# Kernel tuning notes

Hardware: AMD Instinct MI355X
Metric: run time of the kernel (lower is better)

The kernel has to match this reference:

```python
import jax, jax.numpy as jnp
import numpy as np

N = 100000
E = 1000000
F_NODE = 64
F_EDGE = 32
H = 128
C_NODE = 12
C_EDGE = 4


def _glorot(key, shape):
    fan_in, fan_out = shape[0], shape[1]
    s = (6.0 / (fan_in + fan_out)) ** 0.5
    return jax.random.uniform(key, shape, jnp.float32, -s, s)


def setup_inputs() -> dict:
    key = jax.random.key(0)
    ks = jax.random.split(key, 16)
    x = jax.random.normal(ks[0], (N, F_NODE), jnp.float32)
    edge_index = jax.random.randint(ks[1], (2, E), 0, N, jnp.int32)
    edge_attr = jax.random.normal(ks[2], (E, F_EDGE), jnp.float32)
    return {
        "x": x,
        "edge_index": edge_index,
        "edge_attr": edge_attr,
        "We": _glorot(ks[3], (F_NODE, H)), "be": jnp.zeros((H,), jnp.float32),
        "Wc1": _glorot(ks[4], (H, H)), "bc1": jnp.zeros((H,), jnp.float32),
        "Wc2": _glorot(ks[5], (H, H)), "bc2": jnp.zeros((H,), jnp.float32),
        "Wn1": _glorot(ks[6], (H, H // 2)), "bn1": jnp.zeros((H // 2,), jnp.float32),
        "Wn2": _glorot(ks[7], (H // 2, C_NODE)), "bn2": jnp.zeros((C_NODE,), jnp.float32),
        "Wedge1": _glorot(ks[8], (2 * H + F_EDGE, H)), "bedge1": jnp.zeros((H,), jnp.float32),
        "Wedge2": _glorot(ks[9], (H, C_EDGE)), "bedge2": jnp.zeros((C_EDGE,), jnp.float32),
    }


def _gcn_conv(x, W, b, src, tgt, n):
    # PyG GCNConv: add self-loops, symmetric deg normalization, scatter-add.
    xw = x @ W  # [N, H]
    loop = jnp.arange(n, dtype=src.dtype)
    s = jnp.concatenate([src, loop])
    t = jnp.concatenate([tgt, loop])
    deg = jax.ops.segment_sum(jnp.ones_like(t, jnp.float32), t, num_segments=n)
    dinv = jnp.where(deg > 0, jax.lax.rsqrt(jnp.maximum(deg, 1.0)), 0.0)
    norm = dinv[s] * dinv[t]  # [E+N]
    msg = xw[s] * norm[:, None]
    return jax.ops.segment_sum(msg, t, num_segments=n) + b


def reference(x, edge_index, edge_attr, We, be, Wc1, bc1, Wc2, bc2,
              Wn1, bn1, Wn2, bn2, Wedge1, bedge1, Wedge2, bedge2):
    n = x.shape[0]
    row, col = edge_index[0], edge_index[1]
    h = jax.nn.relu(x @ We + be)          # node_embed Linear+ReLU
    h = jax.nn.relu(h)                     # extra F.relu in forward
    h = jax.nn.relu(_gcn_conv(h, Wc1, bc1, row, col, n))
    h = jax.nn.relu(_gcn_conv(h, Wc2, bc2, row, col, n))
    node_logits = jax.nn.relu(h @ Wn1 + bn1) @ Wn2 + bn2
    e = jnp.concatenate([h[row], h[col], edge_attr], axis=-1)  # [E, 2H+Fe]
    edge_logits = jax.nn.relu(e @ Wedge1 + bedge1) @ Wedge2 + bedge2
    return (node_logits, edge_logits)
```

## Files before the change

kernel.cpp:

```cpp
#include <hip/hip_runtime.h>

#define N_NODES 100000
#define N_EDGES 1000000
#define NB_SCAN 391
#define EDGE_OUT_BASE 1200000

typedef __attribute__((ext_vector_type(8))) short short8;
typedef __attribute__((ext_vector_type(4))) unsigned short us4;
typedef __attribute__((ext_vector_type(4))) float f32x4;

__device__ __forceinline__ float bf2f(unsigned short u) {
    unsigned int x = ((unsigned int)u) << 16;
    return __builtin_bit_cast(float, x);
}
__device__ __forceinline__ float lo_bf(unsigned int u) {
    return __builtin_bit_cast(float, u << 16);
}
__device__ __forceinline__ float hi_bf(unsigned int u) {
    return __builtin_bit_cast(float, u & 0xffff0000u);
}
__device__ __forceinline__ unsigned short f2bf(float f) {
    unsigned int x = __builtin_bit_cast(unsigned int, f);
    return (unsigned short)((x + 0x7fffu + ((x >> 16) & 1u)) >> 16);
}

__global__ __launch_bounds__(256) void k_detect(const unsigned short* __restrict__ xr,
                                                int* __restrict__ flag) {
    __shared__ int s[256];
    int t = threadIdx.x;
    int cnt = 0;
    for (int i = t; i < 8192; i += 256) {
        int e = (xr[i] >> 7) & 0xFF;
        if (e >= 148) cnt++;
    }
    s[t] = cnt;
    __syncthreads();
    for (int off = 128; off > 0; off >>= 1) {
        if (t < off) s[t] += s[t + off];
        __syncthreads();
    }
    if (t == 0) *flag = (s[0] > 100) ? 1 : 0;
}

struct WPack { const void* p[14]; };
#define W_TOTAL 87888
__global__ __launch_bounds__(256) void k_convw(WPack wp, const int* __restrict__ flag,
                                               unsigned short* __restrict__ dst) {
    const int starts[15] = {0, 8192, 8320, 24704, 24832, 41216, 41344, 49536,
                            49600, 50368, 50380, 87244, 87372, 87884, 87888};
    bool f32 = (*flag != 0);
    int i = blockIdx.x * 256 + threadIdx.x;
    if (i >= W_TOTAL) return;
    int s = 0;
#pragma unroll
    for (int k = 1; k < 14; k++) s += (i >= starts[k]) ? 1 : 0;
    int j = i - starts[s];
    dst[i] = f32 ? f2bf(((const float*)wp.p[s])[j]) : ((const unsigned short*)wp.p[s])[j];
}
#define OW_We 0
#define OW_be 8192
#define OW_Wc1 8320
#define OW_bc1 24704
#define OW_Wc2 24832
#define OW_bc2 41216
#define OW_Wn1 41344
#define OW_bn1 49536
#define OW_Wn2 49600
#define OW_bn2 50368
#define OW_We1 50380
#define OW_be1 87244
#define OW_We2 87372
#define OW_be2 87884

__global__ __launch_bounds__(256) void k_hist(const int* __restrict__ ecol, int* __restrict__ deg) {
    int e = blockIdx.x * 256 + threadIdx.x;
    if (e < N_EDGES) atomicAdd(&deg[ecol[e]], 1);
}

__global__ __launch_bounds__(256) void k_scanA(const int* __restrict__ deg, int* __restrict__ bsum) {
    __shared__ int s[256];
    int i = blockIdx.x * 256 + threadIdx.x;
    s[threadIdx.x] = (i < N_NODES) ? deg[i] : 0;
    __syncthreads();
    for (int off = 128; off > 0; off >>= 1) {
        if (threadIdx.x < off) s[threadIdx.x] += s[threadIdx.x + off];
        __syncthreads();
    }
    if (threadIdx.x == 0) bsum[blockIdx.x] = s[0];
}

__global__ __launch_bounds__(512) void k_scanB(int* __restrict__ bsum) {
    __shared__ int s[512];
    int t = threadIdx.x;
    int v = (t < NB_SCAN) ? bsum[t] : 0;
    s[t] = v;
    __syncthreads();
    for (int off = 1; off < 512; off <<= 1) {
        int x = (t >= off) ? s[t - off] : 0;
        __syncthreads();
        s[t] += x;
        __syncthreads();
    }
    if (t < NB_SCAN) bsum[t] = s[t] - v;
}

__global__ __launch_bounds__(256) void k_scanC(const int* __restrict__ deg, const int* __restrict__ bsum,
                                               int* __restrict__ row_off, int* __restrict__ cursor,
                                               float* __restrict__ dinv) {
    __shared__ int s[256];
    int i = blockIdx.x * 256 + threadIdx.x;
    int t = threadIdx.x;
    int v = (i < N_NODES) ? deg[i] : 0;
    s[t] = v;
    __syncthreads();
    for (int off = 1; off < 256; off <<= 1) {
        int x = (t >= off) ? s[t - off] : 0;
        __syncthreads();
        s[t] += x;
        __syncthreads();
    }
    int excl = s[t] - v + bsum[blockIdx.x];
    if (i < N_NODES) {
        row_off[i] = excl;
        cursor[i] = excl;
        dinv[i] = rsqrtf((float)(v + 1));
    }
    if (i == N_NODES - 1) row_off[N_NODES] = excl + v;
}

__global__ __launch_bounds__(256) void k_fill(const int* __restrict__ erow, const int* __restrict__ ecol,
                                              int* __restrict__ cursor, int* __restrict__ csr,
                                              int2* __restrict__ aux) {
    int e = blockIdx.x * 256 + threadIdx.x;
    if (e < N_EDGES) {
        int c = ecol[e];
        int pos = atomicAdd(&cursor[c], 1);
        csr[pos] = erow[e];
        aux[pos] = make_int2(e, c);
    }
}

template <int K, int O, bool RELU, bool BIAS, bool SCALE>
__global__ __launch_bounds__(256) void gemm_rows(const void* __restrict__ A, int M,
                                                 const unsigned short* __restrict__ W, int o_real,
                                                 const unsigned short* __restrict__ bias,
                                                 void* __restrict__ Out, int out_pitch,
                                                 const float* __restrict__ rowscale,
                                                 const int* aflag, const int* oflag) {
    constexpr int KP = K + 8;
    constexpr int KS = K / 32;
    constexpr int OT = O / 16;
    __shared__ short wt[O * KP];
    __shared__ float bias_s[O];
    int tid = threadIdx.x;
    for (int idx = tid; idx < K * O; idx += 256) {
        int k = idx / O, o = idx % O;
        short w = 0;
        if (o < o_real) w = (short)W[(size_t)k * o_real + o];
        wt[o * KP + k] = w;
    }
    if (BIAS) {
        for (int o = tid; o < O; o += 256) bias_s[o] = (o < o_real) ? bf2f(bias[o]) : 0.f;
    }
    __syncthreads();

    bool af32 = aflag && (*aflag != 0);
    bool of32 = oflag && (*oflag != 0);

    int wid = tid >> 6, lane = tid & 63;
    int rbase = (blockIdx.x * 4 + wid) * 32;
    if (rbase >= M) return;
    int lq = lane >> 4, lr = lane & 15;

    short8 a[2][KS];
#pragma unroll
    for (int rg = 0; rg < 2; rg++) {
        int row = rbase + rg * 16 + lr;
        if (row >= M) row = M - 1;
        if (af32) {
            const float* ap = (const float*)A + (size_t)row * K + lq * 8;
#pragma unroll
            for (int ks = 0; ks < KS; ks++) {
                f32x4 u0 = *(const f32x4*)(ap + ks * 32);
                f32x4 u1 = *(const f32x4*)(ap + ks * 32 + 4);
                short8 v;
                v[0] = (short)f2bf(u0[0]); v[1] = (short)f2bf(u0[1]);
                v[2] = (short)f2bf(u0[2]); v[3] = (short)f2bf(u0[3]);
                v[4] = (short)f2bf(u1[0]); v[5] = (short)f2bf(u1[1]);
                v[6] = (short)f2bf(u1[2]); v[7] = (short)f2bf(u1[3]);
                a[rg][ks] = v;
            }
        } else {
            const unsigned short* ap = (const unsigned short*)A + (size_t)row * K + lq * 8;
#pragma unroll
            for (int ks = 0; ks < KS; ks++) a[rg][ks] = *(const short8*)(ap + ks * 32);
        }
    }

    f32x4 acc[2][OT];
#pragma unroll
    for (int rg = 0; rg < 2; rg++)
#pragma unroll
        for (int j = 0; j < OT; j++) {
            acc[rg][j][0] = 0.f; acc[rg][j][1] = 0.f; acc[rg][j][2] = 0.f; acc[rg][j][3] = 0.f;
        }

#pragma unroll
    for (int j = 0; j < OT; j++) {
        short8 b[KS];
#pragma unroll
        for (int ks = 0; ks < KS; ks++)
            b[ks] = *(const short8*)(&wt[(lr + 16 * j) * KP + ks * 32 + lq * 8]);
#pragma unroll
        for (int rg = 0; rg < 2; rg++)
#pragma unroll
            for (int ks = 0; ks < KS; ks++)
                acc[rg][j] = __builtin_amdgcn_mfma_f32_16x16x32_bf16(a[rg][ks], b[ks], acc[rg][j], 0, 0, 0);
    }

#pragma unroll
    for (int rg = 0; rg < 2; rg++)
#pragma unroll
        for (int j = 0; j < OT; j++)
#pragma unroll
            for (int r = 0; r < 4; r++) {
                int row = rbase + rg * 16 + lq * 4 + r;
                int col = lr + 16 * j;
                if (row < M && col < o_real) {
                    float v = acc[rg][j][r];
                    if (BIAS) v += bias_s[col];
                    if (RELU) v = fmaxf(v, 0.f);
                    if (SCALE) v *= rowscale[row];
                    size_t oi = (size_t)row * out_pitch + col;
                    if (of32) ((float*)Out)[oi] = v;
                    else ((unsigned short*)Out)[oi] = f2bf(v);
                }
            }
}

__global__ __launch_bounds__(256) void node_head(const unsigned short* __restrict__ A, int M,
                                                 const unsigned short* __restrict__ wbuf,
                                                 void* __restrict__ Out, const int* oflag) {
    __shared__ short wt1[64 * 136];
    __shared__ short zb[128 * 72];
    __shared__ short wt2[16 * 72];
    __shared__ float b1[64];
    __shared__ float b2[16];
    int tid = threadIdx.x;
    const unsigned short* Wn1 = wbuf + OW_Wn1;
    const unsigned short* Wn2 = wbuf + OW_Wn2;
    for (int idx = tid; idx < 64 * 128; idx += 256) {
        int k = idx >> 6, o = idx & 63;
        wt1[o * 136 + k] = (short)Wn1[idx];
    }
    for (int idx = tid; idx < 16 * 64; idx += 256) {
        int o = idx & 15, k = idx >> 4;
        wt2[o * 72 + k] = (o < 12) ? (short)Wn2[k * 12 + o] : 0;
    }
    if (tid < 64) b1[tid] = bf2f(wbuf[OW_bn1 + tid]);
    if (tid < 16) b2[tid] = (tid < 12) ? bf2f(wbuf[OW_bn2 + tid]) : 0.f;
    __syncthreads();

    bool of32 = oflag && (*oflag != 0);
    int wid = tid >> 6, lane = tid & 63;
    int lq = lane >> 4, lr = lane & 15;
    int rbase = blockIdx.x * 128 + wid * 32;

    short8 a[2][4];
#pragma unroll
    for (int rg = 0; rg < 2; rg++) {
        int row = rbase + rg * 16 + lr;
        if (row >= M) row = M - 1;
        const unsigned short* ap = A + (size_t)row * 128 + lq * 8;
#pragma unroll
        for (int ks = 0; ks < 4; ks++) a[rg][ks] = *(const short8*)(ap + ks * 32);
    }

    {
        f32x4 acc[2][4];
#pragma unroll
        for (int rg = 0; rg < 2; rg++)
#pragma unroll
            for (int j = 0; j < 4; j++) {
                acc[rg][j][0] = 0.f; acc[rg][j][1] = 0.f; acc[rg][j][2] = 0.f; acc[rg][j][3] = 0.f;
            }
#pragma unroll
        for (int j = 0; j < 4; j++) {
            short8 b[4];
#pragma unroll
            for (int ks = 0; ks < 4; ks++)
                b[ks] = *(const short8*)(&wt1[(lr + 16 * j) * 136 + ks * 32 + lq * 8]);
#pragma unroll
            for (int rg = 0; rg < 2; rg++)
#pragma unroll
                for (int ks = 0; ks < 4; ks++)
                    acc[rg][j] = __builtin_amdgcn_mfma_f32_16x16x32_bf16(a[rg][ks], b[ks], acc[rg][j], 0, 0, 0);
        }
#pragma unroll
        for (int rg = 0; rg < 2; rg++)
#pragma unroll
            for (int j = 0; j < 4; j++)
#pragma unroll
                for (int r = 0; r < 4; r++) {
                    int rl = wid * 32 + rg * 16 + lq * 4 + r;
                    int col = lr + 16 * j;
                    zb[rl * 72 + col] = (short)f2bf(fmaxf(acc[rg][j][r] + b1[col], 0.f));
                }
    }
    __syncthreads();

    {
        short8 a2[2][2];
#pragma unroll
        for (int rg = 0; rg < 2; rg++) {
            int rl = wid * 32 + rg * 16 + lr;
#pragma unroll
            for (int ks = 0; ks < 2; ks++)
                a2[rg][ks] = *(const short8*)(&zb[rl * 72 + ks * 32 + lq * 8]);
        }
        short8 b[2];
#pragma unroll
        for (int ks = 0; ks < 2; ks++)
            b[ks] = *(const short8*)(&wt2[lr * 72 + ks * 32 + lq * 8]);
        f32x4 acc[2];
#pragma unroll
        for (int rg = 0; rg < 2; rg++) {
            acc[rg][0] = 0.f; acc[rg][1] = 0.f; acc[rg][2] = 0.f; acc[rg][3] = 0.f;
#pragma unroll
            for (int ks = 0; ks < 2; ks++)
                acc[rg] = __builtin_amdgcn_mfma_f32_16x16x32_bf16(a2[rg][ks], b[ks], acc[rg], 0, 0, 0);
        }
#pragma unroll
        for (int rg = 0; rg < 2; rg++)
#pragma unroll
            for (int r = 0; r < 4; r++) {
                int row = rbase + rg * 16 + lq * 4 + r;
                int col = lr;
                if (row < M && col < 12) {
                    float v = acc[rg][r] + b2[col];
                    size_t oi = (size_t)row * 12 + col;
                    if (of32) ((float*)Out)[oi] = v;
                    else ((unsigned short*)Out)[oi] = f2bf(v);
                }
            }
    }
}

__global__ __launch_bounds__(256) void gemm_pq(const unsigned short* __restrict__ A, int M,
                                               const unsigned short* __restrict__ W1,
                                               const unsigned short* __restrict__ W2,
                                               unsigned short* __restrict__ Pout,
                                               unsigned short* __restrict__ Qout) {
    __shared__ short wt[128 * 136];
    int tid = threadIdx.x;
    int wid = tid >> 6, lane = tid & 63;
    int rbase = (blockIdx.x * 4 + wid) * 32;
    int lq = lane >> 4, lr = lane & 15;

    short8 a[2][4];
#pragma unroll
    for (int rg = 0; rg < 2; rg++) {
        int row = rbase + rg * 16 + lr;
        if (row >= M) row = M - 1;
        const unsigned short* ap = A + (size_t)row * 128 + lq * 8;
#pragma unroll
        for (int ks = 0; ks < 4; ks++) a[rg][ks] = *(const short8*)(ap + ks * 32);
    }

    int pc0 = (lr >> 2) * 32 + (lr & 3);

    for (int idx = tid; idx < 128 * 128; idx += 256) {
        int k = idx >> 7, o = idx & 127;
        wt[o * 136 + k] = (short)W1[idx];
    }
    __syncthreads();
    {
        f32x4 acc[2][8];
#pragma unroll
        for (int rg = 0; rg < 2; rg++)
#pragma unroll
            for (int j = 0; j < 8; j++) {
                acc[rg][j][0] = 0.f; acc[rg][j][1] = 0.f; acc[rg][j][2] = 0.f; acc[rg][j][3] = 0.f;
            }
#pragma unroll
        for (int j = 0; j < 8; j++) {
            short8 b[4];
#pragma unroll
            for (int ks = 0; ks < 4; ks++)
                b[ks] = *(const short8*)(&wt[(lr + 16 * j) * 136 + ks * 32 + lq * 8]);
#pragma unroll
            for (int rg = 0; rg < 2; rg++)
#pragma unroll
                for (int ks = 0; ks < 4; ks++)
                    acc[rg][j] = __builtin_amdgcn_mfma_f32_16x16x32_bf16(a[rg][ks], b[ks], acc[rg][j], 0, 0, 0);
        }
#pragma unroll
        for (int rg = 0; rg < 2; rg++)
#pragma unroll
            for (int j = 0; j < 8; j++)
#pragma unroll
                for (int r = 0; r < 4; r++) {
                    int row = rbase + rg * 16 + lq * 4 + r;
                    if (row < M) Pout[(size_t)row * 128 + pc0 + j * 4] = f2bf(acc[rg][j][r]);
                }
    }
    __syncthreads();

    for (int idx = tid; idx < 128 * 128; idx += 256) {
        int k = idx >> 7, o = idx & 127;
        wt[o * 136 + k] = (short)W2[idx];
    }
    __syncthreads();
    {
        f32x4 acc[2][8];
#pragma unroll
        for (int rg = 0; rg < 2; rg++)
#pragma unroll
            for (int j = 0; j < 8; j++) {
                acc[rg][j][0] = 0.f; acc[rg][j][1] = 0.f; acc[rg][j][2] = 0.f; acc[rg][j][3] = 0.f;
            }
#pragma unroll
        for (int j = 0; j < 8; j++) {
            short8 b[4];
#pragma unroll
            for (int ks = 0; ks < 4; ks++)
                b[ks] = *(const short8*)(&wt[(lr + 16 * j) * 136 + ks * 32 + lq * 8]);
#pragma unroll
            for (int rg = 0; rg < 2; rg++)
#pragma unroll
                for (int ks = 0; ks < 4; ks++)
                    acc[rg][j] = __builtin_amdgcn_mfma_f32_16x16x32_bf16(a[rg][ks], b[ks], acc[rg][j], 0, 0, 0);
        }
#pragma unroll
        for (int rg = 0; rg < 2; rg++)
#pragma unroll
            for (int j = 0; j < 8; j++)
#pragma unroll
                for (int r = 0; r < 4; r++) {
                    int row = rbase + rg * 16 + lq * 4 + r;
                    if (row < M) Qout[(size_t)row * 128 + pc0 + j * 4] = f2bf(acc[rg][j][r]);
                }
    }
}

#define CONV_LOADC(U, base)                                                             \
    _Pragma("unroll") for (int k = 0; k < 8; k++) {                                     \
        int p = (base) + k;                                                             \
        int pc = (p < cend) ? p : (cend - 1);                                           \
        int s = csr_src[pc];                                                            \
        U[k] = *(const unsigned int*)(xw_s + (size_t)s * 128 + lane * 2);               \
    }
#define CONV_CONSUME(U, base)                                                           \
    _Pragma("unroll") for (int k = 0; k < 8; k++) {                                     \
        int p = (base) + k;                                                             \
        if (p < cend) {                                                                 \
            float lo = lo_bf(U[k]), hi = hi_bf(U[k]);                                   \
            if (p >= b3)      { A3l += lo; A3h += hi; }                                 \
            else if (p >= b2) { A2l += lo; A2h += hi; }                                 \
            else if (p >= b1) { A1l += lo; A1h += hi; }                                 \
            else              { A0l += lo; A0h += hi; }                                 \
        }                                                                               \
    }
__global__ __launch_bounds__(256) void conv_kernel(const unsigned short* __restrict__ xw_s,
                                                   const int* __restrict__ csr_src,
                                                   const int* __restrict__ row_off,
                                                   const float* __restrict__ dinv,
                                                   const unsigned short* __restrict__ bias,
                                                   unsigned short* __restrict__ out) {
    int wid = threadIdx.x >> 6, lane = threadIdx.x & 63;
    int t0 = (blockIdx.x * 4 + wid) * 4;
    int b0 = row_off[t0], b1 = row_off[t0 + 1], b2 = row_off[t0 + 2];
    int b3 = row_off[t0 + 3], cend = row_off[t0 + 4];

    unsigned int v0 = *(const unsigned int*)(xw_s + (size_t)(t0 + 0) * 128 + lane * 2);
    unsigned int v1 = *(const unsigned int*)(xw_s + (size_t)(t0 + 1) * 128 + lane * 2);
    unsigned int v2 = *(const unsigned int*)(xw_s + (size_t)(t0 + 2) * 128 + lane * 2);
    unsigned int v3 = *(const unsigned int*)(xw_s + (size_t)(t0 + 3) * 128 + lane * 2);
    float A0l = lo_bf(v0), A0h = hi_bf(v0);
    float A1l = lo_bf(v1), A1h = hi_bf(v1);
    float A2l = lo_bf(v2), A2h = hi_bf(v2);
    float A3l = lo_bf(v3), A3h = hi_bf(v3);

    if (b0 < cend) {
        unsigned int UA[8], UB[8];
        int i = b0;
        CONV_LOADC(UA, i);
        while (true) {
            bool hasB = (i + 8) < cend;
            if (hasB) { CONV_LOADC(UB, i + 8); }
            CONV_CONSUME(UA, i);
            i += 8;
            if (!hasB) break;
            bool hasA = (i + 8) < cend;
            if (hasA) { CONV_LOADC(UA, i + 8); }
            CONV_CONSUME(UB, i);
            i += 8;
            if (!hasA) break;
        }
    }

    unsigned int bv = *(const unsigned int*)(bias + lane * 2);
    float bl = lo_bf(bv), bh = hi_bf(bv);
    float d0 = dinv[t0], d1 = dinv[t0 + 1], d2 = dinv[t0 + 2], d3 = dinv[t0 + 3];
    A0l = fmaxf(fmaf(A0l, d0, bl), 0.f); A0h = fmaxf(fmaf(A0h, d0, bh), 0.f);
    A1l = fmaxf(fmaf(A1l, d1, bl), 0.f); A1h = fmaxf(fmaf(A1h, d1, bh), 0.f);
    A2l = fmaxf(fmaf(A2l, d2, bl), 0.f); A2h = fmaxf(fmaf(A2h, d2, bh), 0.f);
    A3l = fmaxf(fmaf(A3l, d3, bl), 0.f); A3h = fmaxf(fmaf(A3h, d3, bh), 0.f);
    *(unsigned int*)(out + (size_t)(t0 + 0) * 128 + lane * 2) =
        (unsigned int)f2bf(A0l) | ((unsigned int)f2bf(A0h) << 16);
    *(unsigned int*)(out + (size_t)(t0 + 1) * 128 + lane * 2) =
        (unsigned int)f2bf(A1l) | ((unsigned int)f2bf(A1h) << 16);
    *(unsigned int*)(out + (size_t)(t0 + 2) * 128 + lane * 2) =
        (unsigned int)f2bf(A2l) | ((unsigned int)f2bf(A2h) << 16);
    *(unsigned int*)(out + (size_t)(t0 + 3) * 128 + lane * 2) =
        (unsigned int)f2bf(A3l) | ((unsigned int)f2bf(A3h) << 16);
}

__device__ __forceinline__ void epi_chunk(f32x4& ov, const f32x4& acc_lo, const f32x4& acc_hi,
                                          short8 pv, short8 qv,
                                          const float* __restrict__ b1s,
                                          const float* __restrict__ w2s, int pb) {
#pragma unroll
    for (int jj = 0; jj < 2; jj++) {
        const f32x4& ac = jj ? acc_hi : acc_lo;
#pragma unroll
        for (int r = 0; r < 4; r++) {
            int idx = jj * 4 + r;
            float t = ac[r] + bf2f((unsigned short)pv[idx]) + bf2f((unsigned short)qv[idx]) + b1s[pb + idx];
            t = fmaxf(t, 0.f);
            f32x4 w2v = *(const f32x4*)(&w2s[(pb + idx) * 4]);
            ov[0] = fmaf(t, w2v[0], ov[0]);
            ov[1] = fmaf(t, w2v[1], ov[1]);
            ov[2] = fmaf(t, w2v[2], ov[2]);
            ov[3] = fmaf(t, w2v[3], ov[3]);
        }
    }
}

__global__ __launch_bounds__(256) void edge_head(const void* __restrict__ ea,
                                                 const int* __restrict__ csr_src,
                                                 const int2* __restrict__ aux,
                                                 const unsigned short* __restrict__ P,
                                                 const unsigned short* __restrict__ Q,
                                                 const unsigned short* __restrict__ wbuf,
                                                 void* __restrict__ out, const int* dtflag) {
    __shared__ short wct[128 * 40];
    __shared__ float w2s[128 * 4];
    __shared__ float b1s[128];
    int tid = threadIdx.x;
    const unsigned short* Wc3 = wbuf + OW_We1 + 256 * 128;
    for (int idx = tid; idx < 32 * 128; idx += 256) {
        int k = idx >> 7, o = idx & 127;
        wct[o * 40 + k] = (short)Wc3[idx];
    }
    for (int idx = tid; idx < 512; idx += 256) {
        int p = idx >> 2, o = idx & 3;
        int ch = 16 * ((p & 31) >> 2) + 4 * (p >> 5) + (p & 3);
        w2s[idx] = bf2f(wbuf[OW_We2 + ch * 4 + o]);
    }
    if (tid < 128) {
        int p = tid;
        int ch = 16 * ((p & 31) >> 2) + 4 * (p >> 5) + (p & 3);
        b1s[p] = bf2f(wbuf[OW_be1 + ch]);
    }
    __syncthreads();

    bool f32io = (*dtflag != 0);
    int wid = tid >> 6, lane = tid & 63;
    int lq = lane >> 4, lr = lane & 15;
    int tbase = (blockIdx.x * 4 + wid) * 2;
    int p0a = tbase * 16, p0b = p0a + 16;

    int posa = p0a + lr, posb = p0b + lr;
    bool va = posa < N_EDGES, vb = posb < N_EDGES;
    int pca = va ? posa : (N_EDGES - 1);
    int pcb = vb ? posb : (N_EDGES - 1);

    int rna = csr_src[pca], rnb = csr_src[pcb];
    int2 axa = aux[pca], axb = aux[pcb];
    int gea = axa.x, cna = axa.y;
    int geb = axb.x, cnb = axb.y;

    auto load_efrag = [&](int ge) -> short8 {
        short8 v;
        if (f32io) {
            const float* eap = (const float*)ea + (size_t)ge * 32 + lq * 8;
            f32x4 u0 = __builtin_nontemporal_load((const f32x4*)eap);
            f32x4 u1 = __builtin_nontemporal_load((const f32x4*)(eap + 4));
            v[0] = (short)f2bf(u0[0]); v[1] = (short)f2bf(u0[1]);
            v[2] = (short)f2bf(u0[2]); v[3] = (short)f2bf(u0[3]);
            v[4] = (short)f2bf(u1[0]); v[5] = (short)f2bf(u1[1]);
            v[6] = (short)f2bf(u1[2]); v[7] = (short)f2bf(u1[3]);
        } else {
            v = __builtin_nontemporal_load((const short8*)((const unsigned short*)ea + (size_t)ge * 32 + lq * 8));
        }
        return v;
    };
    short8 efA = load_efrag(gea);
    short8 efB = load_efrag(geb);

    const unsigned short* PpA = P + (size_t)rna * 128 + lq * 32;
    const unsigned short* QpA = Q + (size_t)cna * 128 + lq * 32;
    const unsigned short* PpB = P + (size_t)rnb * 128 + lq * 32;
    const unsigned short* QpB = Q + (size_t)cnb * 128 + lq * 32;

    f32x4 zero; zero[0] = 0.f; zero[1] = 0.f; zero[2] = 0.f; zero[3] = 0.f;
    f32x4 ovA = zero, ovB = zero;

    {
        short8 pA0 = *(const short8*)(PpA + 0);
        short8 pA1 = *(const short8*)(PpA + 8);
        short8 qA0 = *(const short8*)(QpA + 0);
        short8 qA1 = *(const short8*)(QpA + 8);
        short8 pB0 = *(const short8*)(PpB + 0);
        short8 pB1 = *(const short8*)(PpB + 8);
        short8 qB0 = *(const short8*)(QpB + 0);
        short8 qB1 = *(const short8*)(QpB + 8);
        short8 wf0 = *(const short8*)(&wct[(0 * 16 + lr) * 40 + lq * 8]);
        short8 wf1 = *(const short8*)(&wct[(1 * 16 + lr) * 40 + lq * 8]);
        short8 wf2 = *(const short8*)(&wct[(2 * 16 + lr) * 40 + lq * 8]);
        short8 wf3 = *(const short8*)(&wct[(3 * 16 + lr) * 40 + lq * 8]);
        f32x4 aA0 = __builtin_amdgcn_mfma_f32_16x16x32_bf16(wf0, efA, zero, 0, 0, 0);
        f32x4 aA1 = __builtin_amdgcn_mfma_f32_16x16x32_bf16(wf1, efA, zero, 0, 0, 0);
        f32x4 aA2 = __builtin_amdgcn_mfma_f32_16x16x32_bf16(wf2, efA, zero, 0, 0, 0);
        f32x4 aA3 = __builtin_amdgcn_mfma_f32_16x16x32_bf16(wf3, efA, zero, 0, 0, 0);
        f32x4 aB0 = __builtin_amdgcn_mfma_f32_16x16x32_bf16(wf0, efB, zero, 0, 0, 0);
        f32x4 aB1 = __builtin_amdgcn_mfma_f32_16x16x32_bf16(wf1, efB, zero, 0, 0, 0);
        f32x4 aB2 = __builtin_amdgcn_mfma_f32_16x16x32_bf16(wf2, efB, zero, 0, 0, 0);
        f32x4 aB3 = __builtin_amdgcn_mfma_f32_16x16x32_bf16(wf3, efB, zero, 0, 0, 0);
        epi_chunk(ovA, aA0, aA1, pA0, qA0, b1s, w2s, lq * 32 + 0);
        epi_chunk(ovA, aA2, aA3, pA1, qA1, b1s, w2s, lq * 32 + 8);
        epi_chunk(ovB, aB0, aB1, pB0, qB0, b1s, w2s, lq * 32 + 0);
        epi_chunk(ovB, aB2, aB3, pB1, qB1, b1s, w2s, lq * 32 + 8);
    }
    {
        short8 pA0 = *(const short8*)(PpA + 16);
        short8 pA1 = *(const short8*)(PpA + 24);
        short8 qA0 = *(const short8*)(QpA + 16);
        short8 qA1 = *(const short8*)(QpA + 24);
        short8 pB0 = *(const short8*)(PpB + 16);
        short8 pB1 = *(const short8*)(PpB + 24);
        short8 qB0 = *(const short8*)(QpB + 16);
        short8 qB1 = *(const short8*)(QpB + 24);
        short8 wf0 = *(const short8*)(&wct[(4 * 16 + lr) * 40 + lq * 8]);
        short8 wf1 = *(const short8*)(&wct[(5 * 16 + lr) * 40 + lq * 8]);
        short8 wf2 = *(const short8*)(&wct[(6 * 16 + lr) * 40 + lq * 8]);
        short8 wf3 = *(const short8*)(&wct[(7 * 16 + lr) * 40 + lq * 8]);
        f32x4 aA0 = __builtin_amdgcn_mfma_f32_16x16x32_bf16(wf0, efA, zero, 0, 0, 0);
        f32x4 aA1 = __builtin_amdgcn_mfma_f32_16x16x32_bf16(wf1, efA, zero, 0, 0, 0);
        f32x4 aA2 = __builtin_amdgcn_mfma_f32_16x16x32_bf16(wf2, efA, zero, 0, 0, 0);
        f32x4 aA3 = __builtin_amdgcn_mfma_f32_16x16x32_bf16(wf3, efA, zero, 0, 0, 0);
        f32x4 aB0 = __builtin_amdgcn_mfma_f32_16x16x32_bf16(wf0, efB, zero, 0, 0, 0);
        f32x4 aB1 = __builtin_amdgcn_mfma_f32_16x16x32_bf16(wf1, efB, zero, 0, 0, 0);
        f32x4 aB2 = __builtin_amdgcn_mfma_f32_16x16x32_bf16(wf2, efB, zero, 0, 0, 0);
        f32x4 aB3 = __builtin_amdgcn_mfma_f32_16x16x32_bf16(wf3, efB, zero, 0, 0, 0);
        epi_chunk(ovA, aA0, aA1, pA0, qA0, b1s, w2s, lq * 32 + 16);
        epi_chunk(ovA, aA2, aA3, pA1, qA1, b1s, w2s, lq * 32 + 24);
        epi_chunk(ovB, aB0, aB1, pB0, qB0, b1s, w2s, lq * 32 + 16);
        epi_chunk(ovB, aB2, aB3, pB1, qB1, b1s, w2s, lq * 32 + 24);
    }

#pragma unroll
    for (int c = 0; c < 4; c++) {
        ovA[c] += __shfl_xor(ovA[c], 16);
        ovA[c] += __shfl_xor(ovA[c], 32);
        ovB[c] += __shfl_xor(ovB[c], 16);
        ovB[c] += __shfl_xor(ovB[c], 32);
    }
    if (lq == 0) {
        float be2_0 = bf2f(wbuf[OW_be2 + 0]), be2_1 = bf2f(wbuf[OW_be2 + 1]);
        float be2_2 = bf2f(wbuf[OW_be2 + 2]), be2_3 = bf2f(wbuf[OW_be2 + 3]);
        if (va) {
            size_t oi = (size_t)EDGE_OUT_BASE + (size_t)gea * 4;
            if (f32io) {
                f32x4 res; res[0] = ovA[0] + be2_0; res[1] = ovA[1] + be2_1;
                res[2] = ovA[2] + be2_2; res[3] = ovA[3] + be2_3;
                __builtin_nontemporal_store(res, (f32x4*)((float*)out + oi));
            } else {
                us4 res; res[0] = f2bf(ovA[0] + be2_0); res[1] = f2bf(ovA[1] + be2_1);
                res[2] = f2bf(ovA[2] + be2_2); res[3] = f2bf(ovA[3] + be2_3);
                __builtin_nontemporal_store(res, (us4*)((unsigned short*)out + oi));
            }
        }
        if (vb) {
            size_t oi = (size_t)EDGE_OUT_BASE + (size_t)geb * 4;
            if (f32io) {
                f32x4 res; res[0] = ovB[0] + be2_0; res[1] = ovB[1] + be2_1;
                res[2] = ovB[2] + be2_2; res[3] = ovB[3] + be2_3;
                __builtin_nontemporal_store(res, (f32x4*)((float*)out + oi));
            } else {
                us4 res; res[0] = f2bf(ovB[0] + be2_0); res[1] = f2bf(ovB[1] + be2_1);
                res[2] = f2bf(ovB[2] + be2_2); res[3] = f2bf(ovB[3] + be2_3);
                __builtin_nontemporal_store(res, (us4*)((unsigned short*)out + oi));
            }
        }
    }
}

extern "C" void kernel_launch(void* const* d_in, const int* in_sizes, int n_in,
                              void* d_out, int out_size, void* d_ws, size_t ws_size,
                              hipStream_t stream) {
    const void* x = d_in[0];
    const int* ei = (const int*)d_in[1];
    const void* ea = d_in[2];
    const int* erow = ei;
    const int* ecol = ei + N_EDGES;

    char* ws = (char*)d_ws;
    size_t off = 0;
    auto alloc = [&](size_t bytes) -> void* {
        void* p = ws + off;
        off += (bytes + 255) & ~(size_t)255;
        return p;
    };
    unsigned short* Abuf = (unsigned short*)alloc((size_t)N_NODES * 128 * 2);
    unsigned short* Bbuf = (unsigned short*)alloc((size_t)N_NODES * 128 * 2);
    int* deg = (int*)alloc((size_t)N_NODES * 4);
    int* row_off = (int*)alloc((size_t)(N_NODES + 1) * 4);
    int* cursor = (int*)alloc((size_t)N_NODES * 4);
    int* csr = (int*)alloc((size_t)N_EDGES * 4);
    int2* aux = (int2*)alloc((size_t)N_EDGES * 8);
    int* bsum = (int*)alloc(512 * 4);
    float* dinv = (float*)alloc((size_t)N_NODES * 4);
    unsigned short* wbuf = (unsigned short*)alloc((size_t)W_TOTAL * 2);
    int* dtflag = (int*)alloc(256);

    k_detect<<<1, 256, 0, stream>>>((const unsigned short*)x, dtflag);

    WPack wp;
    for (int i = 0; i < 14; i++) wp.p[i] = d_in[3 + i];
    k_convw<<<(W_TOTAL + 255) / 256, 256, 0, stream>>>(wp, dtflag, wbuf);

    (void)hipMemsetAsync(deg, 0, (size_t)N_NODES * 4, stream);
    k_hist<<<(N_EDGES + 255) / 256, 256, 0, stream>>>(ecol, deg);
    k_scanA<<<NB_SCAN, 256, 0, stream>>>(deg, bsum);
    k_scanB<<<1, 512, 0, stream>>>(bsum);
    k_scanC<<<NB_SCAN, 256, 0, stream>>>(deg, bsum, row_off, cursor, dinv);
    k_fill<<<(N_EDGES + 255) / 256, 256, 0, stream>>>(erow, ecol, cursor, csr, aux);

    int gB = (N_NODES + 127) / 128;
    gemm_rows<64, 128, true, true, false><<<gB, 256, 0, stream>>>(x, N_NODES, wbuf + OW_We, 128, wbuf + OW_be, Abuf, 128, nullptr, dtflag, nullptr);
    gemm_rows<128, 128, false, false, true><<<gB, 256, 0, stream>>>(Abuf, N_NODES, wbuf + OW_Wc1, 128, nullptr, Bbuf, 128, dinv, nullptr, nullptr);
    conv_kernel<<<N_NODES / 16, 256, 0, stream>>>(Bbuf, csr, row_off, dinv, wbuf + OW_bc1, Abuf);
    gemm_rows<128, 128, false, false, true><<<gB, 256, 0, stream>>>(Abuf, N_NODES, wbuf + OW_Wc2, 128, nullptr, Bbuf, 128, dinv, nullptr, nullptr);
    conv_kernel<<<N_NODES / 16, 256, 0, stream>>>(Bbuf, csr, row_off, dinv, wbuf + OW_bc2, Abuf);
    node_head<<<gB, 256, 0, stream>>>(Abuf, N_NODES, wbuf, d_out, dtflag);
    gemm_pq<<<gB, 256, 0, stream>>>(Abuf, N_NODES, wbuf + OW_We1, wbuf + OW_We1 + 128 * 128, Bbuf, Abuf);
    edge_head<<<(N_EDGES + 127) / 128, 256, 0, stream>>>(ea, csr, aux, Bbuf, Abuf, wbuf, d_out, dtflag);
}
```

Baseline: 547.8 us.

## Restructure GCN aggregation to one node per wave with 16-byte gathers

The conv aggregation kernel now assigns one target node per wavefront instead of four. Each quarter-wave gathers a different neighbor row using 16-byte short8 loads, and the neighbor indices are loaded once and broadcast with shuffles. A cross-quarter xor-shuffle reduction combines the partial sums before the epilogue. This aims to cut per-row load instructions and increase memory-level parallelism. The cost is a reduction step, idle lanes for low-degree nodes, and a launch with four times as many blocks.

```diff
diff --git a/kernel.cpp b/kernel.cpp
--- a/kernel.cpp
+++ b/kernel.cpp
@@ -443,24 +443,6 @@
     }
 }
 
-#define CONV_LOADC(U, base)                                                             \
-    _Pragma("unroll") for (int k = 0; k < 8; k++) {                                     \
-        int p = (base) + k;                                                             \
-        int pc = (p < cend) ? p : (cend - 1);                                           \
-        int s = csr_src[pc];                                                            \
-        U[k] = *(const unsigned int*)(xw_s + (size_t)s * 128 + lane * 2);               \
-    }
-#define CONV_CONSUME(U, base)                                                           \
-    _Pragma("unroll") for (int k = 0; k < 8; k++) {                                     \
-        int p = (base) + k;                                                             \
-        if (p < cend) {                                                                 \
-            float lo = lo_bf(U[k]), hi = hi_bf(U[k]);                                   \
-            if (p >= b3)      { A3l += lo; A3h += hi; }                                 \
-            else if (p >= b2) { A2l += lo; A2h += hi; }                                 \
-            else if (p >= b1) { A1l += lo; A1h += hi; }                                 \
-            else              { A0l += lo; A0h += hi; }                                 \
-        }                                                                               \
-    }
 __global__ __launch_bounds__(256) void conv_kernel(const unsigned short* __restrict__ xw_s,
                                                    const int* __restrict__ csr_src,
                                                    const int* __restrict__ row_off,
@@ -468,52 +450,55 @@
                                                    const unsigned short* __restrict__ bias,
                                                    unsigned short* __restrict__ out) {
     int wid = threadIdx.x >> 6, lane = threadIdx.x & 63;
-    int t0 = (blockIdx.x * 4 + wid) * 4;
-    int b0 = row_off[t0], b1 = row_off[t0 + 1], b2 = row_off[t0 + 2];
-    int b3 = row_off[t0 + 3], cend = row_off[t0 + 4];
-
-    unsigned int v0 = *(const unsigned int*)(xw_s + (size_t)(t0 + 0) * 128 + lane * 2);
-    unsigned int v1 = *(const unsigned int*)(xw_s + (size_t)(t0 + 1) * 128 + lane * 2);
-    unsigned int v2 = *(const unsigned int*)(xw_s + (size_t)(t0 + 2) * 128 + lane * 2);
-    unsigned int v3 = *(const unsigned int*)(xw_s + (size_t)(t0 + 3) * 128 + lane * 2);
-    float A0l = lo_bf(v0), A0h = hi_bf(v0);
-    float A1l = lo_bf(v1), A1h = hi_bf(v1);
-    float A2l = lo_bf(v2), A2h = hi_bf(v2);
-    float A3l = lo_bf(v3), A3h = hi_bf(v3);
-
-    if (b0 < cend) {
-        unsigned int UA[8], UB[8];
-        int i = b0;
-        CONV_LOADC(UA, i);
-        while (true) {
-            bool hasB = (i + 8) < cend;
-            if (hasB) { CONV_LOADC(UB, i + 8); }
-            CONV_CONSUME(UA, i);
-            i += 8;
-            if (!hasB) break;
-            bool hasA = (i + 8) < cend;
-            if (hasA) { CONV_LOADC(UA, i + 8); }
-            CONV_CONSUME(UB, i);
-            i += 8;
-            if (!hasA) break;
-        }
-    }
-
-    unsigned int bv = *(const unsigned int*)(bias + lane * 2);
-    float bl = lo_bf(bv), bh = hi_bf(bv);
-    float d0 = dinv[t0], d1 = dinv[t0 + 1], d2 = dinv[t0 + 2], d3 = dinv[t0 + 3];
-    A0l = fmaxf(fmaf(A0l, d0, bl), 0.f); A0h = fmaxf(fmaf(A0h, d0, bh), 0.f);
-    A1l = fmaxf(fmaf(A1l, d1, bl), 0.f); A1h = fmaxf(fmaf(A1h, d1, bh), 0.f);
-    A2l = fmaxf(fmaf(A2l, d2, bl), 0.f); A2h = fmaxf(fmaf(A2h, d2, bh), 0.f);
-    A3l = fmaxf(fmaf(A3l, d3, bl), 0.f); A3h = fmaxf(fmaf(A3h, d3, bh), 0.f);
-    *(unsigned int*)(out + (size_t)(t0 + 0) * 128 + lane * 2) =
-        (unsigned int)f2bf(A0l) | ((unsigned int)f2bf(A0h) << 16);
-    *(unsigned int*)(out + (size_t)(t0 + 1) * 128 + lane * 2) =
-        (unsigned int)f2bf(A1l) | ((unsigned int)f2bf(A1h) << 16);
-    *(unsigned int*)(out + (size_t)(t0 + 2) * 128 + lane * 2) =
-        (unsigned int)f2bf(A2l) | ((unsigned int)f2bf(A2h) << 16);
-    *(unsigned int*)(out + (size_t)(t0 + 3) * 128 + lane * 2) =
-        (unsigned int)f2bf(A3l) | ((unsigned int)f2bf(A3h) << 16);
+    int t = blockIdx.x * 4 + wid;
+    int beg = row_off[t], end = row_off[t + 1];
+    int d = end - beg;
+    int q = lane >> 4, lr = lane & 15;
+
+    int myidx = (lane < d) ? csr_src[beg + lane] : 0;
+
+    float acc[8];
+#pragma unroll
+    for (int c = 0; c < 8; c++) acc[c] = 0.f;
+
+    for (int i = 0; i < d; i += 8) {
+        int p0 = i + q, p1 = i + 4 + q;
+        bool ok0 = p0 < d, ok1 = p1 < d;
+        int s0 = (p0 < 64) ? __shfl(myidx, p0) : (ok0 ? csr_src[beg + p0] : 0);
+        int s1 = (p1 < 64) ? __shfl(myidx, p1) : (ok1 ? csr_src[beg + p1] : 0);
+        if (!ok0) s0 = 0;
+        if (!ok1) s1 = 0;
+        short8 v0 = *(const short8*)(xw_s + (size_t)s0 * 128 + lr * 8);
+        short8 v1 = *(const short8*)(xw_s + (size_t)s1 * 128 + lr * 8);
+        if (ok0) {
+#pragma unroll
+            for (int c = 0; c < 8; c++) acc[c] += bf2f((unsigned short)v0[c]);
+        }
+        if (ok1) {
+#pragma unroll
+            for (int c = 0; c < 8; c++) acc[c] += bf2f((unsigned short)v1[c]);
+        }
+    }
+
+#pragma unroll
+    for (int c = 0; c < 8; c++) {
+        acc[c] += __shfl_xor(acc[c], 16);
+        acc[c] += __shfl_xor(acc[c], 32);
+    }
+
+    short8 sv = *(const short8*)(xw_s + (size_t)t * 128 + lr * 8);
+    short8 bv = *(const short8*)(bias + lr * 8);
+    float dt = dinv[t];
+    if (q == 0) {
+        short8 o;
+#pragma unroll
+        for (int c = 0; c < 8; c++) {
+            float v = acc[c] + bf2f((unsigned short)sv[c]);
+            v = fmaxf(fmaf(v, dt, bf2f((unsigned short)bv[c])), 0.f);
+            o[c] = (short)f2bf(v);
+        }
+        *(short8*)(out + (size_t)t * 128 + lr * 8) = o;
+    }
 }
 
 __device__ __forceinline__ void epi_chunk(f32x4& ov, const f32x4& acc_lo, const f32x4& acc_hi,
@@ -741,9 +726,9 @@
     int gB = (N_NODES + 127) / 128;
     gemm_rows<64, 128, true, true, false><<<gB, 256, 0, stream>>>(x, N_NODES, wbuf + OW_We, 128, wbuf + OW_be, Abuf, 128, nullptr, dtflag, nullptr);
     gemm_rows<128, 128, false, false, true><<<gB, 256, 0, stream>>>(Abuf, N_NODES, wbuf + OW_Wc1, 128, nullptr, Bbuf, 128, dinv, nullptr, nullptr);
-    conv_kernel<<<N_NODES / 16, 256, 0, stream>>>(Bbuf, csr, row_off, dinv, wbuf + OW_bc1, Abuf);
+    conv_kernel<<<N_NODES / 4, 256, 0, stream>>>(Bbuf, csr, row_off, dinv, wbuf + OW_bc1, Abuf);
     gemm_rows<128, 128, false, false, true><<<gB, 256, 0, stream>>>(Abuf, N_NODES, wbuf + OW_Wc2, 128, nullptr, Bbuf, 128, dinv, nullptr, nullptr);
-    conv_kernel<<<N_NODES / 16, 256, 0, stream>>>(Bbuf, csr, row_off, dinv, wbuf + OW_bc2, Abuf);
+    conv_kernel<<<N_NODES / 4, 256, 0, stream>>>(Bbuf, csr, row_off, dinv, wbuf + OW_bc2, Abuf);
     node_head<<<gB, 256, 0, stream>>>(Abuf, N_NODES, wbuf, d_out, dtflag);
     gemm_pq<<<gB, 256, 0, stream>>>(Abuf, N_NODES, wbuf + OW_We1, wbuf + OW_We1 + 128 * 128, Bbuf, Abuf);
     edge_head<<<(N_EDGES + 127) / 128, 256, 0, stream>>>(ea, csr, aux, Bbuf, Abuf, wbuf, d_out, dtflag);
```

After: 528.5 us. -3.5%, faster.
